# Optimization experiments

Hardware: AMD Instinct MI355X
Metric: run time of the kernel (lower is better)

## Reference

```python
import jax, jax.numpy as jnp
import numpy as np

B, L, H = 4, 96, 512
R, T = 257, 21


def setup_inputs() -> dict:
    key = jax.random.key(0)
    ks = jax.random.split(key, 7)
    std_in = (2.0 / (H + 1 + R)) ** 0.5  # xavier_normal over [H+1, R]
    return {
        "layer1": jax.random.normal(ks[0], (B, L, H), jnp.float32),
        "layer2": jax.random.normal(ks[1], (B, L, H), jnp.float32),
        "layer3": jax.random.normal(ks[2], (B, L, H), jnp.float32),
        "W_1": jax.random.normal(ks[3], (H + 1, R), jnp.float32) * std_in,
        "W_2": jax.random.normal(ks[4], (H + 1, R), jnp.float32) * std_in,
        "W_3": jax.random.normal(ks[5], (H + 1, R), jnp.float32) * std_in,
        "W_l": jax.random.normal(ks[6], (1, R, T), jnp.float32),
    }


def reference(layer1, layer2, layer3, W_1, W_2, W_3, W_l):
    # Append bias-ones feature, as in the torch forward.
    ones = jnp.ones((*layer1.shape[:2], 1), layer1.dtype)
    l1 = jnp.concatenate([layer1, ones], axis=-1)  # [n, i, H+1]
    l2 = jnp.concatenate([layer2, ones], axis=-1)  # [n, j, H+1]
    l3 = jnp.concatenate([layer3, jnp.ones((*layer3.shape[:-1], 1), layer3.dtype)], axis=-1)
    # Factor the CP contraction: project each stream to rank space first.
    p1 = jnp.einsum("nia,ar->nir", l1, W_1)  # [n, i, r]
    p2 = jnp.einsum("njb,br->njr", l2, W_2)  # [n, j, r]
    p3 = jnp.einsum("nkc,cr->nkr", l3, W_3)  # [n, k, r]
    # Fold label map into one stream, then rank-reduce outer product.
    p3t = jnp.einsum("nkr,rt->ntkr", p3, W_l[0])  # [n, t, k, r]
    out = jnp.einsum("nir,njr,ntkr->ntijk", p1, p2, p3t)  # [n, t, i, j, k]
    return out
```

## Files before the change

### kernel.cpp

```cpp
#include <hip/hip_runtime.h>
#include <hip/hip_bf16.h>

#define RR 257
#define RP 288
#define TT 21

typedef __attribute__((ext_vector_type(4))) float f32x4;
typedef __attribute__((ext_vector_type(8))) short bf16x8;

union Pack8 { unsigned short s[8]; uint4 v; };

__device__ __forceinline__ unsigned short f2b(float f) {
    union { float f; unsigned u; } v; v.f = f;
    unsigned r = v.u + 0x7fffu + ((v.u >> 16) & 1u);
    return (unsigned short)(r >> 16);
}

__global__ __launch_bounds__(384) void proj_kernel(
    const float* __restrict__ l1, const float* __restrict__ l2, const float* __restrict__ l3,
    const float* __restrict__ W1, const float* __restrict__ W2, const float* __restrict__ W3,
    float* __restrict__ P1f, float* __restrict__ P2f, float* __restrict__ P3f)
{
    int bx = blockIdx.x;
    int grp = bx % 48;
    int n = (bx / 48) & 3;
    int s = bx / 192;
    const float* layer = (s == 0) ? l1 : (s == 1) ? l2 : l3;
    const float* W     = (s == 0) ? W1 : (s == 1) ? W2 : W3;
    int i0 = grp * 2;

    __shared__ __attribute__((aligned(16))) float x[1024];
    const float4* src = (const float4*)(layer + (n * 96 + i0) * 512);
    float4* xv = (float4*)x;
    for (int idx = threadIdx.x; idx < 256; idx += 384) xv[idx] = src[idx];
    __syncthreads();

    int r = threadIdx.x;
    if (r < RP) {
        float a0 = 0.f, a1 = 0.f;
        if (r < RR) {
            float b = W[512 * RR + r];
            a0 = a1 = b;
            #pragma unroll 8
            for (int a = 0; a < 512; ++a) {
                float wa = W[a * RR + r];
                a0 = fmaf(x[a], wa, a0);
                a1 = fmaf(x[512 + a], wa, a1);
            }
        }
        float* P = (s == 0) ? P1f : (s == 1) ? P2f : P3f;
        int base = (n * 96 + i0) * RP + r;
        P[base]      = a0;
        P[base + RP] = a1;
    }
}

__global__ __launch_bounds__(256) void prep_kernel(
    const float* __restrict__ P1f, const float* __restrict__ P2f,
    const float* __restrict__ P3f, const float* __restrict__ Wl,
    unsigned short* __restrict__ Af, unsigned short* __restrict__ Bf)
{
    int bx = blockIdx.x;
    if (bx < 384) {
        int n = bx / 96, i = bx % 96;
        __shared__ __attribute__((aligned(16))) float p1row[RP];
        for (int r = threadIdx.x; r < RP; r += 256)
            p1row[r] = P1f[(n * 96 + i) * RP + r];
        __syncthreads();

        unsigned short* dst = Af + (size_t)(n * 576 + i * 6) * 9 * 512;
        for (int idx = threadIdx.x; idx < 3456; idx += 256) {
            int L = idx & 63;
            int rest = idx >> 6;
            int ks = rest % 9, rgl = rest / 9;
            int j = rgl * 16 + (L & 15);
            int k8 = ks * 32 + (L >> 4) * 8;
            const float* p2p = P2f + (n * 96 + j) * RP + k8;
            float4 b0 = *(const float4*)(p2p);
            float4 b1 = *(const float4*)(p2p + 4);
            float4 a0 = *(const float4*)(p1row + k8);
            float4 a1 = *(const float4*)(p1row + k8 + 4);
            Pack8 u;
            u.s[0] = f2b(a0.x * b0.x); u.s[1] = f2b(a0.y * b0.y);
            u.s[2] = f2b(a0.z * b0.z); u.s[3] = f2b(a0.w * b0.w);
            u.s[4] = f2b(a1.x * b1.x); u.s[5] = f2b(a1.y * b1.y);
            u.s[6] = f2b(a1.z * b1.z); u.s[7] = f2b(a1.w * b1.w);
            *(uint4*)(dst + (size_t)(rgl * 9 + ks) * 512 + L * 8) = u.v;
        }
    } else {
        int b2 = bx - 384;
        int h = b2 & 1;
        int t = (b2 >> 1) % TT, n = b2 / (2 * TT);
        __shared__ __attribute__((aligned(16))) float wl_lds[RP];
        for (int r = threadIdx.x; r < RP; r += 256)
            wl_lds[r] = (r < RR) ? Wl[r * TT + t] : 0.f;
        __syncthreads();

        unsigned short* dst = Bf + (size_t)(n * TT + t) * 6 * 9 * 512;
        for (int idx2 = threadIdx.x; idx2 < 1728; idx2 += 256) {
            int idx = h * 1728 + idx2;
            int L = idx & 63;
            int rest = idx >> 6;
            int ks = rest % 9, kg = rest / 9;
            int col = kg * 16 + (L & 15);
            int r8 = ks * 32 + (L >> 4) * 8;
            const float* p3p = P3f + (n * 96 + col) * RP + r8;
            float4 p0 = *(const float4*)(p3p);
            float4 p1 = *(const float4*)(p3p + 4);
            float4 w0 = *(const float4*)(wl_lds + r8);
            float4 w1 = *(const float4*)(wl_lds + r8 + 4);
            Pack8 u;
            u.s[0] = f2b(p0.x * w0.x); u.s[1] = f2b(p0.y * w0.y);
            u.s[2] = f2b(p0.z * w0.z); u.s[3] = f2b(p0.w * w0.w);
            u.s[4] = f2b(p1.x * w1.x); u.s[5] = f2b(p1.y * w1.y);
            u.s[6] = f2b(p1.z * w1.z); u.s[7] = f2b(p1.w * w1.w);
            *(uint4*)(dst + (size_t)(kg * 9 + ks) * 512 + L * 8) = u.v;
        }
    }
}

#define LOADA(s, kss) { _Pragma("unroll") for (int mf = 0; mf < 4; ++mf) \
    fa[s][mf] = *(const bf16x8*)(abase + (mf * 9 + (kss)) * 512); }
#define LOADB(s, kss) { _Pragma("unroll") for (int nf = 0; nf < 6; ++nf) \
    fb[s][nf] = *(const bf16x8*)(bbase + (nf * 9 + (kss)) * 512); }
#define MFMAS(s) { _Pragma("unroll") for (int mf = 0; mf < 4; ++mf) { \
    _Pragma("unroll") for (int nf = 0; nf < 6; ++nf) \
      acc[mf][nf] = __builtin_amdgcn_mfma_f32_16x16x32_bf16(fb[s][nf], fa[s][mf], acc[mf][nf], 0, 0, 0); } }

__global__ __launch_bounds__(64, 2) void tri12_kernel(
    const unsigned short* __restrict__ Af, const unsigned short* __restrict__ Bf,
    float* __restrict__ out)
{
    int orig = blockIdx.x;
    if (orig < 2048) {
        int key = ((orig >> 3) ^ (orig >> 8)) & 7;
        for (int d = 0; d < key; ++d) __builtin_amdgcn_s_sleep(16);
    }
    int bx = (orig & 7) * 1512 + (orig >> 3);
    int t = bx % TT;
    int mtn = bx / TT;
    int mt = mtn % 144;
    int n = mtn / 144;

    int lane = threadIdx.x & 63;

    const unsigned short* abase =
        Af + (size_t)(n * 576 + mt * 4) * 9 * 512 + lane * 8;
    const unsigned short* bbase =
        Bf + (size_t)(n * TT + t) * 27648 + lane * 8;

    f32x4 acc[4][6] = {};
    bf16x8 fa[2][4], fb[2][6];

    LOADA(0, 0); LOADB(0, 0);
    #pragma unroll
    for (int kp = 0; kp < 4; ++kp) {
        LOADA(1, 2 * kp + 1); LOADB(1, 2 * kp + 1);
        MFMAS(0);
        LOADA(0, 2 * kp + 2); LOADB(0, 2 * kp + 2);
        MFMAS(1);
    }
    MFMAS(0);

    __shared__ __attribute__((aligned(16))) float tb[1600];
    int Llo = lane & 15, Lhi = lane >> 4;
    size_t outbase = ((size_t)(n * TT + t) * 9216 + mt * 64) * 96;

    #pragma unroll
    for (int mf = 0; mf < 4; ++mf) {
        #pragma unroll
        for (int nf = 0; nf < 6; ++nf)
            *(f32x4*)&tb[Llo * 100 + nf * 16 + Lhi * 4] = acc[mf][nf];
        float* gdst = out + outbase + (size_t)mf * 16 * 96;
        #pragma unroll
        for (int q = 0; q < 6; ++q) {
            int fidx = q * 64 + lane;
            int ml = fidx / 24, k4 = fidx % 24;
            f32x4 vv = *(const f32x4*)&tb[ml * 100 + k4 * 4];
            __builtin_nontemporal_store(vv, (f32x4*)(gdst + (size_t)fidx * 4));
        }
    }
}

extern "C" void kernel_launch(void* const* d_in, const int* in_sizes, int n_in,
                              void* d_out, int out_size, void* d_ws, size_t ws_size,
                              hipStream_t stream) {
    const float* l1 = (const float*)d_in[0];
    const float* l2 = (const float*)d_in[1];
    const float* l3 = (const float*)d_in[2];
    const float* W1 = (const float*)d_in[3];
    const float* W2 = (const float*)d_in[4];
    const float* W3 = (const float*)d_in[5];
    const float* Wl = (const float*)d_in[6];

    float* P1f = (float*)d_ws;
    float* P2f = P1f + 384 * RP;
    float* P3f = P2f + 384 * RP;
    unsigned short* Af = (unsigned short*)(P3f + 384 * RP);
    unsigned short* Bf = Af + (size_t)4 * 576 * 9 * 512;

    proj_kernel<<<576, 384, 0, stream>>>(l1, l2, l3, W1, W2, W3, P1f, P2f, P3f);
    prep_kernel<<<552, 256, 0, stream>>>(P1f, P2f, P3f, Wl, Af, Bf);
    tri12_kernel<<<12096, 64, 0, stream>>>(Af, Bf, (float*)d_out);
}
```

Before: 112.2 us.

## Fuse prep into main kernel, forming bf16 fragments on the fly from fp32 projections

Removes the separate prep kernel and the materialized bf16 A/B buffers. The projection kernel now writes P2/P3 directly in MFMA fragment layout. The main kernel uses 4-wave blocks that build the W_l-scaled P3 tile in LDS once per block and compute the P1*P2 Hadamard products in registers with packed bf16 conversion before each MFMA. This cuts one launch and a large round trip of intermediate data through global memory, at the cost of extra VALU work and LDS usage per block, which may lower occupancy.

```diff
diff --git a/kernel.cpp b/kernel.cpp
--- a/kernel.cpp
+++ b/kernel.cpp
@@ -9,11 +9,18 @@
 typedef __attribute__((ext_vector_type(8))) short bf16x8;
 
 union Pack8 { unsigned short s[8]; uint4 v; };
+union FragU { unsigned w[4]; bf16x8 v; };
 
 __device__ __forceinline__ unsigned short f2b(float f) {
     union { float f; unsigned u; } v; v.f = f;
     unsigned r = v.u + 0x7fffu + ((v.u >> 16) & 1u);
     return (unsigned short)(r >> 16);
+}
+
+__device__ __forceinline__ unsigned cvtpk(float lo, float hi) {
+    unsigned r;
+    asm("v_cvt_pk_bf16_f32 %0, %1, %2" : "=v"(r) : "v"(lo), "v"(hi));
+    return r;
 }
 
 __global__ __launch_bounds__(384) void proj_kernel(
@@ -48,87 +55,51 @@
                 a1 = fmaf(x[512 + a], wa, a1);
             }
         }
-        float* P = (s == 0) ? P1f : (s == 1) ? P2f : P3f;
-        int base = (n * 96 + i0) * RP + r;
-        P[base]      = a0;
-        P[base + RP] = a1;
-    }
-}
-
-__global__ __launch_bounds__(256) void prep_kernel(
+        if (s == 0) {
+            int base = (n * 96 + i0) * RP + r;
+            P1f[base]      = a0;
+            P1f[base + RP] = a1;
+        } else {
+            float* P = (s == 1) ? P2f : P3f;
+            int ks = r >> 5, hi = (r >> 3) & 3, e = r & 7;
+            #pragma unroll
+            for (int q = 0; q < 2; ++q) {
+                int row = i0 + q;
+                int rg = row >> 4, Llo = row & 15;
+                P[(size_t)((n * 6 + rg) * 9 + ks) * 512 + (hi * 16 + Llo) * 8 + e]
+                    = q ? a1 : a0;
+            }
+        }
+    }
+}
+
+#define LOADP(s, kss) { \
+    _Pragma("unroll") for (int q = 0; q < 3; ++q) { \
+        const float* pp = p2base + (size_t)(q * 9 + (kss)) * 512; \
+        rp2[s][q][0] = *(const f32x4*)(pp); \
+        rp2[s][q][1] = *(const f32x4*)(pp + 4); } \
+    rp1[s][0] = *(const f32x4*)(p1base + (kss) * 32); \
+    rp1[s][1] = *(const f32x4*)(p1base + (kss) * 32 + 4); }
+
+#define CONV(s) { \
+    _Pragma("unroll") for (int q = 0; q < 3; ++q) { \
+        f32x4 h0 = rp1[s][0] * rp2[s][q][0]; \
+        f32x4 h1 = rp1[s][1] * rp2[s][q][1]; \
+        FragU u; \
+        u.w[0] = cvtpk(h0[0], h0[1]); u.w[1] = cvtpk(h0[2], h0[3]); \
+        u.w[2] = cvtpk(h1[0], h1[1]); u.w[3] = cvtpk(h1[2], h1[3]); \
+        fa[q] = u.v; } }
+
+#define LOADFB(kss) { _Pragma("unroll") for (int nf = 0; nf < 6; ++nf) \
+    fb[nf] = *(const bf16x8*)(lbase + (nf * 9 + (kss)) * 512); }
+
+#define MFMAS() { _Pragma("unroll") for (int mf = 0; mf < 3; ++mf) { \
+    _Pragma("unroll") for (int nf = 0; nf < 6; ++nf) \
+      acc[mf][nf] = __builtin_amdgcn_mfma_f32_16x16x32_bf16(fb[nf], fa[mf], acc[mf][nf], 0, 0, 0); } }
+
+__global__ __launch_bounds__(256, 2) void tri13_kernel(
     const float* __restrict__ P1f, const float* __restrict__ P2f,
     const float* __restrict__ P3f, const float* __restrict__ Wl,
-    unsigned short* __restrict__ Af, unsigned short* __restrict__ Bf)
-{
-    int bx = blockIdx.x;
-    if (bx < 384) {
-        int n = bx / 96, i = bx % 96;
-        __shared__ __attribute__((aligned(16))) float p1row[RP];
-        for (int r = threadIdx.x; r < RP; r += 256)
-            p1row[r] = P1f[(n * 96 + i) * RP + r];
-        __syncthreads();
-
-        unsigned short* dst = Af + (size_t)(n * 576 + i * 6) * 9 * 512;
-        for (int idx = threadIdx.x; idx < 3456; idx += 256) {
-            int L = idx & 63;
-            int rest = idx >> 6;
-            int ks = rest % 9, rgl = rest / 9;
-            int j = rgl * 16 + (L & 15);
-            int k8 = ks * 32 + (L >> 4) * 8;
-            const float* p2p = P2f + (n * 96 + j) * RP + k8;
-            float4 b0 = *(const float4*)(p2p);
-            float4 b1 = *(const float4*)(p2p + 4);
-            float4 a0 = *(const float4*)(p1row + k8);
-            float4 a1 = *(const float4*)(p1row + k8 + 4);
-            Pack8 u;
-            u.s[0] = f2b(a0.x * b0.x); u.s[1] = f2b(a0.y * b0.y);
-            u.s[2] = f2b(a0.z * b0.z); u.s[3] = f2b(a0.w * b0.w);
-            u.s[4] = f2b(a1.x * b1.x); u.s[5] = f2b(a1.y * b1.y);
-            u.s[6] = f2b(a1.z * b1.z); u.s[7] = f2b(a1.w * b1.w);
-            *(uint4*)(dst + (size_t)(rgl * 9 + ks) * 512 + L * 8) = u.v;
-        }
-    } else {
-        int b2 = bx - 384;
-        int h = b2 & 1;
-        int t = (b2 >> 1) % TT, n = b2 / (2 * TT);
-        __shared__ __attribute__((aligned(16))) float wl_lds[RP];
-        for (int r = threadIdx.x; r < RP; r += 256)
-            wl_lds[r] = (r < RR) ? Wl[r * TT + t] : 0.f;
-        __syncthreads();
-
-        unsigned short* dst = Bf + (size_t)(n * TT + t) * 6 * 9 * 512;
-        for (int idx2 = threadIdx.x; idx2 < 1728; idx2 += 256) {
-            int idx = h * 1728 + idx2;
-            int L = idx & 63;
-            int rest = idx >> 6;
-            int ks = rest % 9, kg = rest / 9;
-            int col = kg * 16 + (L & 15);
-            int r8 = ks * 32 + (L >> 4) * 8;
-            const float* p3p = P3f + (n * 96 + col) * RP + r8;
-            float4 p0 = *(const float4*)(p3p);
-            float4 p1 = *(const float4*)(p3p + 4);
-            float4 w0 = *(const float4*)(wl_lds + r8);
-            float4 w1 = *(const float4*)(wl_lds + r8 + 4);
-            Pack8 u;
-            u.s[0] = f2b(p0.x * w0.x); u.s[1] = f2b(p0.y * w0.y);
-            u.s[2] = f2b(p0.z * w0.z); u.s[3] = f2b(p0.w * w0.w);
-            u.s[4] = f2b(p1.x * w1.x); u.s[5] = f2b(p1.y * w1.y);
-            u.s[6] = f2b(p1.z * w1.z); u.s[7] = f2b(p1.w * w1.w);
-            *(uint4*)(dst + (size_t)(kg * 9 + ks) * 512 + L * 8) = u.v;
-        }
-    }
-}
-
-#define LOADA(s, kss) { _Pragma("unroll") for (int mf = 0; mf < 4; ++mf) \
-    fa[s][mf] = *(const bf16x8*)(abase + (mf * 9 + (kss)) * 512); }
-#define LOADB(s, kss) { _Pragma("unroll") for (int nf = 0; nf < 6; ++nf) \
-    fb[s][nf] = *(const bf16x8*)(bbase + (nf * 9 + (kss)) * 512); }
-#define MFMAS(s) { _Pragma("unroll") for (int mf = 0; mf < 4; ++mf) { \
-    _Pragma("unroll") for (int nf = 0; nf < 6; ++nf) \
-      acc[mf][nf] = __builtin_amdgcn_mfma_f32_16x16x32_bf16(fb[s][nf], fa[s][mf], acc[mf][nf], 0, 0, 0); } }
-
-__global__ __launch_bounds__(64, 2) void tri12_kernel(
-    const unsigned short* __restrict__ Af, const unsigned short* __restrict__ Bf,
     float* __restrict__ out)
 {
     int orig = blockIdx.x;
@@ -136,38 +107,69 @@
         int key = ((orig >> 3) ^ (orig >> 8)) & 7;
         for (int d = 0; d < key; ++d) __builtin_amdgcn_s_sleep(16);
     }
-    int bx = (orig & 7) * 1512 + (orig >> 3);
+    int bx = (orig & 7) * 504 + (orig >> 3);
     int t = bx % TT;
     int mtn = bx / TT;
-    int mt = mtn % 144;
-    int n = mtn / 144;
-
-    int lane = threadIdx.x & 63;
-
-    const unsigned short* abase =
-        Af + (size_t)(n * 576 + mt * 4) * 9 * 512 + lane * 8;
-    const unsigned short* bbase =
-        Bf + (size_t)(n * TT + t) * 27648 + lane * 8;
-
-    f32x4 acc[4][6] = {};
-    bf16x8 fa[2][4], fb[2][6];
-
-    LOADA(0, 0); LOADB(0, 0);
+    int mt = mtn % 48;
+    int n = mtn / 48;
+
+    int tid = threadIdx.x, lane = tid & 63, wv = tid >> 6;
+
+    __shared__ __attribute__((aligned(16))) unsigned short blds[27648];
+    __shared__ __attribute__((aligned(16))) float tbuf[4][1600];
+    __shared__ __attribute__((aligned(16))) float wl_lds[RP];
+
+    for (int r = tid; r < RP; r += 256)
+        wl_lds[r] = (r < RR) ? Wl[r * TT + t] : 0.f;
+    __syncthreads();
+
+    for (int idx = tid; idx < 3456; idx += 256) {
+        int L = idx & 63;
+        int rest = idx >> 6;
+        int ks = rest % 9, kg = rest / 9;
+        const float* pp = P3f + (size_t)((n * 6 + kg) * 9 + ks) * 512 + L * 8;
+        float4 p0 = *(const float4*)(pp);
+        float4 p1v = *(const float4*)(pp + 4);
+        int r0 = ks * 32 + (L >> 4) * 8;
+        float4 w0 = *(const float4*)(wl_lds + r0);
+        float4 w1 = *(const float4*)(wl_lds + r0 + 4);
+        Pack8 u;
+        u.s[0] = f2b(p0.x * w0.x); u.s[1] = f2b(p0.y * w0.y);
+        u.s[2] = f2b(p0.z * w0.z); u.s[3] = f2b(p0.w * w0.w);
+        u.s[4] = f2b(p1v.x * w1.x); u.s[5] = f2b(p1v.y * w1.y);
+        u.s[6] = f2b(p1v.z * w1.z); u.s[7] = f2b(p1v.w * w1.w);
+        *(uint4*)(blds + (size_t)(kg * 9 + ks) * 512 + L * 8) = u.v;
+    }
+    __syncthreads();
+
+    int i = 2 * mt + (wv >> 1);
+    int rgj = (wv & 1) * 3;
+    const float* p2base = P2f + (size_t)((n * 6 + rgj) * 9) * 512 + lane * 8;
+    const float* p1base = P1f + (size_t)(n * 96 + i) * RP + (lane >> 4) * 8;
+    const unsigned short* lbase = blds + lane * 8;
+
+    f32x4 acc[3][6] = {};
+    f32x4 rp2[2][3][2], rp1[2][2];
+    bf16x8 fa[3], fb[6];
+
+    LOADP(0, 0);
     #pragma unroll
-    for (int kp = 0; kp < 4; ++kp) {
-        LOADA(1, 2 * kp + 1); LOADB(1, 2 * kp + 1);
-        MFMAS(0);
-        LOADA(0, 2 * kp + 2); LOADB(0, 2 * kp + 2);
-        MFMAS(1);
-    }
-    MFMAS(0);
-
-    __shared__ __attribute__((aligned(16))) float tb[1600];
+    for (int ks = 0; ks < 9; ++ks) {
+        int cur = ks & 1, nxt = cur ^ 1;
+        if (ks < 8) {
+            if (cur) { LOADP(0, ks + 1); } else { LOADP(1, ks + 1); }
+        }
+        if (cur) { CONV(1); } else { CONV(0); }
+        LOADFB(ks);
+        MFMAS();
+    }
+
+    float* tb = tbuf[wv];
     int Llo = lane & 15, Lhi = lane >> 4;
-    size_t outbase = ((size_t)(n * TT + t) * 9216 + mt * 64) * 96;
+    size_t outbase = ((size_t)(n * TT + t) * 9216 + mt * 192 + wv * 48) * 96;
 
     #pragma unroll
-    for (int mf = 0; mf < 4; ++mf) {
+    for (int mf = 0; mf < 3; ++mf) {
         #pragma unroll
         for (int nf = 0; nf < 6; ++nf)
             *(f32x4*)&tb[Llo * 100 + nf * 16 + Lhi * 4] = acc[mf][nf];
@@ -195,11 +197,8 @@
 
     float* P1f = (float*)d_ws;
     float* P2f = P1f + 384 * RP;
-    float* P3f = P2f + 384 * RP;
-    unsigned short* Af = (unsigned short*)(P3f + 384 * RP);
-    unsigned short* Bf = Af + (size_t)4 * 576 * 9 * 512;
+    float* P3f = P2f + 4 * 6 * 9 * 512;
 
     proj_kernel<<<576, 384, 0, stream>>>(l1, l2, l3, W1, W2, W3, P1f, P2f, P3f);
-    prep_kernel<<<552, 256, 0, stream>>>(P1f, P2f, P3f, Wl, Af, Bf);
-    tri12_kernel<<<12096, 64, 0, stream>>>(Af, Bf, (float*)d_out);
-}
+    tri13_kernel<<<4032, 256, 0, stream>>>(P1f, P2f, P3f, Wl, (float*)d_out);
+}
```

Result: slower. 177.4 us (+58.2%).
